# Performance work log

Measured on AMD Instinct MI355X. Metric: run time of the kernel, lower is better.

## Reference

```python
import jax, jax.numpy as jnp
import numpy as np

N = 100000          # num nodes
E = 1600000         # num edges
IN_F = 256
OUT_F = 256
D_LABEL = 32
ALPHA = 0.2         # LeakyReLU negative slope
EPS = 1e-9


def setup_inputs() -> dict:
    key = jax.random.key(0)
    k1, k2, k3, k4 = jax.random.split(key, 4)
    h = jax.random.normal(k1, (N, IN_F), dtype=jnp.float32)
    label = jax.random.normal(k2, (N, D_LABEL), dtype=jnp.float32)
    # xavier_uniform with gain=1.414 on [IN_F, OUT_F]
    limit = 1.414 * np.sqrt(6.0 / (IN_F + OUT_F))
    W = jax.random.uniform(k3, (IN_F, OUT_F), dtype=jnp.float32,
                           minval=-limit, maxval=limit)
    adj_indices = jax.random.randint(k4, (2, E), 0, N, dtype=jnp.int64)
    return {"h": h, "label": label, "W": W, "adj_indices": adj_indices}


def reference(h, label, W, adj_indices):
    src = adj_indices[0]  # [E]
    dst = adj_indices[1]  # [E]
    Wh = h @ W  # [N, OUT_F]
    # edge attention logits: leakyrelu(<label[src], label[dst]>)
    e = jnp.sum(label[src] * label[dst], axis=1)            # [E]
    e = jnp.where(e >= 0, e, ALPHA * e)                     # LeakyReLU
    # segment softmax over rows (src)
    exp_e = jnp.exp(e)                                      # [E]
    row_sum = jax.ops.segment_sum(exp_e, src, num_segments=N)  # [N]
    row_sum = jnp.maximum(row_sum, EPS)
    att = exp_e / row_sum[src]                              # [E]
    # dropout is identity at inference (training=False)
    # sparse-dense matmul: h_prime[i] = sum_{(i,j) in edges} att * Wh[j]
    msgs = att[:, None] * Wh[dst]                           # [E, OUT_F]
    h_prime = jax.ops.segment_sum(msgs, src, num_segments=N)  # [N, OUT_F]
    return h_prime  # concat=False -> no ELU
```

## Files before the change

### kernel.cpp

```cpp
#include <hip/hip_runtime.h>
#include <hip/hip_bf16.h>

#define NNODES 100000
#define NEDGES 1600000
#define ALPHA  0.2f
#define EPSV   1e-9f

typedef __bf16 bf16x8 __attribute__((ext_vector_type(8)));
typedef float  f32x4  __attribute__((ext_vector_type(4)));
typedef unsigned short u16x8 __attribute__((ext_vector_type(8)));

static __device__ inline unsigned short f2bf(float f) {
    unsigned int u = __float_as_uint(f);
    unsigned int r = u + 0x7fff + ((u >> 16) & 1);
    return (unsigned short)(r >> 16);
}
static __device__ inline float bf2f(unsigned short v) {
    return __uint_as_float((unsigned int)v << 16);
}

__global__ void k_init(const float* __restrict__ W, unsigned short* __restrict__ Wt,
                       unsigned int* __restrict__ head) {
    const int i = blockIdx.x * 256 + threadIdx.x;
    if (i < NNODES) head[i] = 0xFFFFFFFFu;
    if (i < 65536) {
        const int n = i >> 8, k = i & 255;
        Wt[i] = f2bf(W[k * 256 + n]);
    }
}

#define BM 128
#define BK 32
#define LSTRIDE 40
__global__ __launch_bounds__(256, 2) void k_gemm(const float* __restrict__ h,
                                                 const unsigned short* __restrict__ Wt,
                                                 unsigned short* __restrict__ Wh) {
    __shared__ __align__(16) unsigned short As[BM * LSTRIDE];
    __shared__ __align__(16) unsigned short Bs[256 * LSTRIDE];
    const int tid  = threadIdx.x;
    const int m0   = blockIdx.x * BM;
    const int wave = tid >> 6;
    const int lane = tid & 63;
    const int wm = (wave & 1) * 64;
    const int wn = (wave >> 1) * 128;
    const int fm = lane & 15;
    const int fq = lane >> 4;
    const int fk = fq * 8;

    f32x4 acc[4][8];
    const f32x4 z = {0.f, 0.f, 0.f, 0.f};
#pragma unroll
    for (int i = 0; i < 4; ++i)
#pragma unroll
        for (int j = 0; j < 8; ++j) acc[i][j] = z;

    const int arow = tid >> 1;
    const int acol = (tid & 1) * 16;
    const bool arow_ok = (m0 + arow) < NNODES;
    const float* hrow = h + (size_t)(m0 + arow) * 256 + acol;

    for (int kc = 0; kc < 256; kc += BK) {
        float4 a0, a1, a2, a3;
        if (arow_ok) {
            a0 = *(const float4*)(hrow + kc + 0);
            a1 = *(const float4*)(hrow + kc + 4);
            a2 = *(const float4*)(hrow + kc + 8);
            a3 = *(const float4*)(hrow + kc + 12);
        } else {
            a0 = a1 = a2 = a3 = make_float4(0.f, 0.f, 0.f, 0.f);
        }
        u16x8 bv[4];
#pragma unroll
        for (int q = 0; q < 4; ++q) {
            const int c = tid + 256 * q;
            const int n = c >> 2, koff = (c & 3) * 8;
            bv[q] = *(const u16x8*)(Wt + n * 256 + kc + koff);
        }
        __syncthreads();
        u16x8 p0, p1;
        p0[0]=f2bf(a0.x); p0[1]=f2bf(a0.y); p0[2]=f2bf(a0.z); p0[3]=f2bf(a0.w);
        p0[4]=f2bf(a1.x); p0[5]=f2bf(a1.y); p0[6]=f2bf(a1.z); p0[7]=f2bf(a1.w);
        p1[0]=f2bf(a2.x); p1[1]=f2bf(a2.y); p1[2]=f2bf(a2.z); p1[3]=f2bf(a2.w);
        p1[4]=f2bf(a3.x); p1[5]=f2bf(a3.y); p1[6]=f2bf(a3.z); p1[7]=f2bf(a3.w);
        *(u16x8*)&As[arow * LSTRIDE + acol]     = p0;
        *(u16x8*)&As[arow * LSTRIDE + acol + 8] = p1;
#pragma unroll
        for (int q = 0; q < 4; ++q) {
            const int c = tid + 256 * q;
            const int n = c >> 2, koff = (c & 3) * 8;
            *(u16x8*)&Bs[n * LSTRIDE + koff] = bv[q];
        }
        __syncthreads();
        bf16x8 af[4], bfr[8];
#pragma unroll
        for (int i = 0; i < 4; ++i)
            af[i] = __builtin_bit_cast(bf16x8,
                *(const u16x8*)&As[(wm + 16 * i + fm) * LSTRIDE + fk]);
#pragma unroll
        for (int j = 0; j < 8; ++j)
            bfr[j] = __builtin_bit_cast(bf16x8,
                *(const u16x8*)&Bs[(wn + 16 * j + fm) * LSTRIDE + fk]);
#pragma unroll
        for (int i = 0; i < 4; ++i)
#pragma unroll
            for (int j = 0; j < 8; ++j)
                acc[i][j] = __builtin_amdgcn_mfma_f32_16x16x32_bf16(af[i], bfr[j], acc[i][j], 0, 0, 0);
    }
#pragma unroll
    for (int i = 0; i < 4; ++i) {
#pragma unroll
        for (int r = 0; r < 4; ++r) {
            const int grow = m0 + wm + 16 * i + fq * 4 + r;
            if (grow < NNODES) {
                unsigned short* orow = Wh + (size_t)grow * 256 + wn + fm;
#pragma unroll
                for (int j = 0; j < 8; ++j)
                    orow[16 * j] = f2bf(acc[i][j][r]);
            }
        }
    }
}

__global__ __launch_bounds__(256) void k_attn_chain(const float* __restrict__ label,
                                                    const int* __restrict__ src,
                                                    const int* __restrict__ dst,
                                                    unsigned int* __restrict__ head,
                                                    uint4* __restrict__ rec) {
    const int t = blockIdx.x * 256 + threadIdx.x;
    const int e = t >> 2;
    const int l4 = t & 3;
    if (e >= NEDGES) return;
    const int s = src[e], d = dst[e];
    const float4* ls = (const float4*)&label[s * 32 + l4 * 8];
    const float4* ld = (const float4*)&label[d * 32 + l4 * 8];
    const float4 a0 = ls[0], a1 = ls[1];
    const float4 b0 = ld[0], b1 = ld[1];
    float dot = a0.x * b0.x + a0.y * b0.y + a0.z * b0.z + a0.w * b0.w
              + a1.x * b1.x + a1.y * b1.y + a1.z * b1.z + a1.w * b1.w;
    dot += __shfl_xor(dot, 1);
    dot += __shfl_xor(dot, 2);
    if (l4 == 0) {
        const float lr = dot >= 0.f ? dot : ALPHA * dot;
        const float w = expf(lr);
        const unsigned int old = atomicExch(&head[s], (unsigned int)e);
        rec[e] = make_uint4(old, (unsigned int)d, __float_as_uint(w), 0u);
    }
}

__global__ __launch_bounds__(256) void k_aggregate(const unsigned short* __restrict__ Wh,
                                                   const unsigned int* __restrict__ head,
                                                   const uint4* __restrict__ rec,
                                                   float* __restrict__ out) {
    const int node = blockIdx.x * 8 + (threadIdx.x >> 5);
    if (node >= NNODES) return;
    const int sub = threadIdx.x & 31;
    const unsigned short* __restrict__ Whc = Wh + sub * 8;
    float acc[8] = {0.f, 0.f, 0.f, 0.f, 0.f, 0.f, 0.f, 0.f};
    float wsum = 0.f;
    unsigned int cur = head[node];
    while (cur != 0xFFFFFFFFu) {
        const uint4 p = rec[cur];
        const u16x8 v = *(const u16x8*)&Whc[(size_t)p.y * 256];
        const float w = __uint_as_float(p.z);
        wsum += w;
#pragma unroll
        for (int c = 0; c < 8; ++c) acc[c] = fmaf(w, bf2f(v[c]), acc[c]);
        cur = p.x;
    }
    const float inv = 1.f / fmaxf(wsum, EPSV);
    float4 o0 = make_float4(acc[0] * inv, acc[1] * inv, acc[2] * inv, acc[3] * inv);
    float4 o1 = make_float4(acc[4] * inv, acc[5] * inv, acc[6] * inv, acc[7] * inv);
    float* orow = out + (size_t)node * 256 + sub * 8;
    *(float4*)(orow + 0) = o0;
    *(float4*)(orow + 4) = o1;
}

extern "C" void kernel_launch(void* const* d_in, const int* in_sizes, int n_in,
                              void* d_out, int out_size, void* d_ws, size_t ws_size,
                              hipStream_t stream) {
    const float* h     = (const float*)d_in[0];
    const float* label = (const float*)d_in[1];
    const float* W     = (const float*)d_in[2];
    const int*   adj   = (const int*)d_in[3];
    const int* src = adj;
    const int* dst = adj + NEDGES;
    float* out = (float*)d_out;

    char* ws = (char*)d_ws;
    unsigned short* Wh   = (unsigned short*)(ws + 0);
    unsigned short* Wt   = (unsigned short*)(ws + 51200000);
    uint4*        rec    = (uint4*)        (ws + 51400000);
    unsigned int* head   = (unsigned int*) (ws + 77000000);

    k_init<<<392, 256, 0, stream>>>(W, Wt, head);
    k_gemm<<<(NNODES + BM - 1) / BM, 256, 0, stream>>>(h, Wt, Wh);
    k_attn_chain<<<(4 * NEDGES + 255) / 256, 256, 0, stream>>>(label, src, dst, head, rec);
    k_aggregate<<<(NNODES + 7) / 8, 256, 0, stream>>>(Wh, head, rec, out);
}
```

Measured before the change: 419.7 us.

## Fuse edge attention computation into aggregation and shrink edge records

Moves the label dot product, LeakyReLU and exp from a separate per-edge kernel into the aggregation loop. The source label row is loaded once per node and each destination label row is read alongside its Wh row. The chain-building kernel now writes 8-byte records (next, dst) instead of 16-byte ones. This removes a full pass over the edges with random label gathers and halves record traffic. In exchange, aggregation does extra label gathers and shuffle reductions on its latency-bound linked-list walk.

```diff
diff --git a/kernel.cpp b/kernel.cpp
--- a/kernel.cpp
+++ b/kernel.cpp
@@ -27,6 +27,17 @@
         const int n = i >> 8, k = i & 255;
         Wt[i] = f2bf(W[k * 256 + n]);
     }
+}
+
+__global__ __launch_bounds__(256) void k_chain(const int* __restrict__ src,
+                                               const int* __restrict__ dst,
+                                               unsigned int* __restrict__ head,
+                                               uint2* __restrict__ rec) {
+    const int e = blockIdx.x * 256 + threadIdx.x;
+    if (e >= NEDGES) return;
+    const int s = src[e];
+    const unsigned int old = atomicExch(&head[s], (unsigned int)e);
+    rec[e] = make_uint2(old, (unsigned int)dst[e]);
 }
 
 #define BM 128
@@ -121,47 +132,33 @@
     }
 }
 
-__global__ __launch_bounds__(256) void k_attn_chain(const float* __restrict__ label,
-                                                    const int* __restrict__ src,
-                                                    const int* __restrict__ dst,
-                                                    unsigned int* __restrict__ head,
-                                                    uint4* __restrict__ rec) {
-    const int t = blockIdx.x * 256 + threadIdx.x;
-    const int e = t >> 2;
-    const int l4 = t & 3;
-    if (e >= NEDGES) return;
-    const int s = src[e], d = dst[e];
-    const float4* ls = (const float4*)&label[s * 32 + l4 * 8];
-    const float4* ld = (const float4*)&label[d * 32 + l4 * 8];
-    const float4 a0 = ls[0], a1 = ls[1];
-    const float4 b0 = ld[0], b1 = ld[1];
-    float dot = a0.x * b0.x + a0.y * b0.y + a0.z * b0.z + a0.w * b0.w
-              + a1.x * b1.x + a1.y * b1.y + a1.z * b1.z + a1.w * b1.w;
-    dot += __shfl_xor(dot, 1);
-    dot += __shfl_xor(dot, 2);
-    if (l4 == 0) {
-        const float lr = dot >= 0.f ? dot : ALPHA * dot;
-        const float w = expf(lr);
-        const unsigned int old = atomicExch(&head[s], (unsigned int)e);
-        rec[e] = make_uint4(old, (unsigned int)d, __float_as_uint(w), 0u);
-    }
-}
-
-__global__ __launch_bounds__(256) void k_aggregate(const unsigned short* __restrict__ Wh,
-                                                   const unsigned int* __restrict__ head,
-                                                   const uint4* __restrict__ rec,
-                                                   float* __restrict__ out) {
+__global__ __launch_bounds__(256) void k_agg(const unsigned short* __restrict__ Wh,
+                                             const float* __restrict__ label,
+                                             const unsigned int* __restrict__ head,
+                                             const uint2* __restrict__ rec,
+                                             float* __restrict__ out) {
     const int node = blockIdx.x * 8 + (threadIdx.x >> 5);
     if (node >= NNODES) return;
     const int sub = threadIdx.x & 31;
+    const int c4 = (sub & 7) * 4;
     const unsigned short* __restrict__ Whc = Wh + sub * 8;
+
+    const float4 lsv = *(const float4*)&label[(size_t)node * 32 + c4];
+
     float acc[8] = {0.f, 0.f, 0.f, 0.f, 0.f, 0.f, 0.f, 0.f};
     float wsum = 0.f;
     unsigned int cur = head[node];
     while (cur != 0xFFFFFFFFu) {
-        const uint4 p = rec[cur];
-        const u16x8 v = *(const u16x8*)&Whc[(size_t)p.y * 256];
-        const float w = __uint_as_float(p.z);
+        const uint2 p = rec[cur];
+        const unsigned int d = p.y;
+        const float4 ldv = *(const float4*)&label[(size_t)d * 32 + c4];
+        const u16x8 v = *(const u16x8*)&Whc[(size_t)d * 256];
+        float dot = lsv.x * ldv.x + lsv.y * ldv.y + lsv.z * ldv.z + lsv.w * ldv.w;
+        dot += __shfl_xor(dot, 1);
+        dot += __shfl_xor(dot, 2);
+        dot += __shfl_xor(dot, 4);
+        const float lr = fmaxf(dot, ALPHA * dot);
+        const float w = expf(lr);
         wsum += w;
 #pragma unroll
         for (int c = 0; c < 8; ++c) acc[c] = fmaf(w, bf2f(v[c]), acc[c]);
@@ -189,11 +186,11 @@
     char* ws = (char*)d_ws;
     unsigned short* Wh   = (unsigned short*)(ws + 0);
     unsigned short* Wt   = (unsigned short*)(ws + 51200000);
-    uint4*        rec    = (uint4*)        (ws + 51400000);
-    unsigned int* head   = (unsigned int*) (ws + 77000000);
+    uint2*        rec    = (uint2*)        (ws + 51400000);
+    unsigned int* head   = (unsigned int*) (ws + 64200000);
 
     k_init<<<392, 256, 0, stream>>>(W, Wt, head);
+    k_chain<<<(NEDGES + 255) / 256, 256, 0, stream>>>(src, dst, head, rec);
     k_gemm<<<(NNODES + BM - 1) / BM, 256, 0, stream>>>(h, Wt, Wh);
-    k_attn_chain<<<(4 * NEDGES + 255) / 256, 256, 0, stream>>>(label, src, dst, head, rec);
-    k_aggregate<<<(NNODES + 7) / 8, 256, 0, stream>>>(Wh, head, rec, out);
+    k_agg<<<(NNODES + 7) / 8, 256, 0, stream>>>(Wh, label, head, rec, out);
 }
```

After: 449.0 us. 7.0% more time.

## Pack edge records into 8 bytes and pad head array to separate cache lines

Applied to the files above, without the earlier changes.

Edge linked-list records shrink from 16-byte uint4 to 8-byte uint2 by packing a 21-bit next index, a 17-bit destination and a 26-bit truncated exp weight, which halves record write and read traffic. The head array is padded so each node's atomic slot sits 64 bytes apart, reducing atomic contention and false sharing on shared lines. In exchange the init kernel must now fill a 16x larger head array, and the weight loses its low mantissa bits.

```diff
diff --git a/kernel.cpp b/kernel.cpp
--- a/kernel.cpp
+++ b/kernel.cpp
@@ -6,6 +6,9 @@
 #define ALPHA  0.2f
 #define EPSV   1e-9f
 
+#define HPAD   16
+#define SENT21 0x1FFFFFu
+
 typedef __bf16 bf16x8 __attribute__((ext_vector_type(8)));
 typedef float  f32x4  __attribute__((ext_vector_type(4)));
 typedef unsigned short u16x8 __attribute__((ext_vector_type(8)));
@@ -22,7 +25,7 @@
 __global__ void k_init(const float* __restrict__ W, unsigned short* __restrict__ Wt,
                        unsigned int* __restrict__ head) {
     const int i = blockIdx.x * 256 + threadIdx.x;
-    if (i < NNODES) head[i] = 0xFFFFFFFFu;
+    if (i < NNODES * HPAD) head[i] = 0xFFFFFFFFu;
     if (i < 65536) {
         const int n = i >> 8, k = i & 255;
         Wt[i] = f2bf(W[k * 256 + n]);
@@ -125,7 +128,7 @@
                                                     const int* __restrict__ src,
                                                     const int* __restrict__ dst,
                                                     unsigned int* __restrict__ head,
-                                                    uint4* __restrict__ rec) {
+                                                    uint2* __restrict__ rec) {
     const int t = blockIdx.x * 256 + threadIdx.x;
     const int e = t >> 2;
     const int l4 = t & 3;
@@ -142,14 +145,18 @@
     if (l4 == 0) {
         const float lr = dot >= 0.f ? dot : ALPHA * dot;
         const float w = expf(lr);
-        const unsigned int old = atomicExch(&head[s], (unsigned int)e);
-        rec[e] = make_uint4(old, (unsigned int)d, __float_as_uint(w), 0u);
+        const unsigned int w26 = __float_as_uint(w) >> 6;
+        const unsigned int wlo = w26 & 0x7FFu;
+        const unsigned int whi = w26 >> 11;
+        const unsigned int old = atomicExch(&head[(size_t)s * HPAD], (unsigned int)e);
+        const unsigned int nxt = old & SENT21;
+        rec[e] = make_uint2(nxt | (wlo << 21), (unsigned int)d | (whi << 17));
     }
 }
 
 __global__ __launch_bounds__(256) void k_aggregate(const unsigned short* __restrict__ Wh,
                                                    const unsigned int* __restrict__ head,
-                                                   const uint4* __restrict__ rec,
+                                                   const uint2* __restrict__ rec,
                                                    float* __restrict__ out) {
     const int node = blockIdx.x * 8 + (threadIdx.x >> 5);
     if (node >= NNODES) return;
@@ -157,15 +164,17 @@
     const unsigned short* __restrict__ Whc = Wh + sub * 8;
     float acc[8] = {0.f, 0.f, 0.f, 0.f, 0.f, 0.f, 0.f, 0.f};
     float wsum = 0.f;
-    unsigned int cur = head[node];
-    while (cur != 0xFFFFFFFFu) {
-        const uint4 p = rec[cur];
-        const u16x8 v = *(const u16x8*)&Whc[(size_t)p.y * 256];
-        const float w = __uint_as_float(p.z);
+    unsigned int cur = head[(size_t)node * HPAD] & SENT21;
+    while (cur != SENT21) {
+        const uint2 p = rec[cur];
+        const unsigned int d   = p.y & 0x1FFFFu;
+        const unsigned int w26 = ((p.y >> 17) << 11) | (p.x >> 21);
+        const float w = __uint_as_float(w26 << 6);
+        const u16x8 v = *(const u16x8*)&Whc[(size_t)d * 256];
         wsum += w;
 #pragma unroll
         for (int c = 0; c < 8; ++c) acc[c] = fmaf(w, bf2f(v[c]), acc[c]);
-        cur = p.x;
+        cur = p.x & SENT21;
     }
     const float inv = 1.f / fmaxf(wsum, EPSV);
     float4 o0 = make_float4(acc[0] * inv, acc[1] * inv, acc[2] * inv, acc[3] * inv);
@@ -189,10 +198,10 @@
     char* ws = (char*)d_ws;
     unsigned short* Wh   = (unsigned short*)(ws + 0);
     unsigned short* Wt   = (unsigned short*)(ws + 51200000);
-    uint4*        rec    = (uint4*)        (ws + 51400000);
-    unsigned int* head   = (unsigned int*) (ws + 77000000);
-
-    k_init<<<392, 256, 0, stream>>>(W, Wt, head);
+    uint2*        rec    = (uint2*)        (ws + 51400000);
+    unsigned int* head   = (unsigned int*) (ws + 64200000);
+
+    k_init<<<(NNODES * HPAD + 255) / 256, 256, 0, stream>>>(W, Wt, head);
     k_gemm<<<(NNODES + BM - 1) / BM, 256, 0, stream>>>(h, Wt, Wh);
     k_attn_chain<<<(4 * NEDGES + 255) / 256, 256, 0, stream>>>(label, src, dst, head, rec);
     k_aggregate<<<(NNODES + 7) / 8, 256, 0, stream>>>(Wh, head, rec, out);
```

Result: no change. 425.2 us (+1.3%).
